# Optimization experiments

Hardware: AMD Instinct MI355X
Metric: run time of the kernel (lower is better)

Reference implementation:

```python
import jax, jax.numpy as jnp
import numpy as np

BS = 16; N_PER = 1024; N = BS * N_PER; K = 9; E = N * K
H = 128; NODE_D = 64; EDGE_D = 16; RBF_DIM = 20; R_CUT = 1.0; L = 4; SF = 0.1


def setup_inputs():
    ks = jax.random.split(jax.random.key(0), 24)
    X = jax.random.normal(ks[0], (N, 3), dtype=jnp.float32) * 0.5
    node_attr = jax.random.normal(ks[1], (N, NODE_D), dtype=jnp.float32)
    edge_attr = jax.random.normal(ks[2], (E, EDGE_D), dtype=jnp.float32)
    idx = jnp.arange(N, dtype=jnp.int32)
    bid = idx // N_PER
    Seg = ((idx % N_PER) >= (N_PER // 2)).astype(jnp.int32)
    row = jnp.repeat(idx, K)
    col = (row // N_PER) * N_PER + jax.random.randint(ks[3], (E,), 0, N_PER, dtype=jnp.int32)
    edges = jnp.stack([row, col])

    def g(k, shape, fan):
        return jax.random.normal(k, shape, dtype=jnp.float32) * (1.0 / float(np.sqrt(fan)))

    MI = 2 * H + RBF_DIM + EDGE_D  # message MLP input dim
    return {
        'X': X, 'node_attr': node_attr, 'edge_attr': edge_attr,
        'W_in1': g(ks[4], (NODE_D, H), NODE_D), 'b_in1': jnp.zeros((H,), jnp.float32),
        'W_in2': g(ks[5], (H, H), H), 'b_in2': jnp.zeros((H,), jnp.float32),
        'We1': g(ks[6], (L, MI, H), MI), 'be1': jnp.zeros((L, H), jnp.float32),
        'We2': g(ks[7], (L, H, H), H), 'be2': jnp.zeros((L, H), jnp.float32),
        'Wv': g(ks[8], (L, H, H), H), 'Wvv': g(ks[9], (L, H, H), H),
        'Wh1': g(ks[10], (L, 2 * H, H), 2 * H), 'bh1': jnp.zeros((L, H), jnp.float32),
        'Wh2': g(ks[11], (L, H, H), H), 'bh2': jnp.zeros((L, H), jnp.float32),
        'Wi1': g(ks[12], (L, H, H), H), 'bi1': jnp.zeros((L, H), jnp.float32),
        'Wi2': g(ks[13], (L, H, H), H), 'bi2': jnp.zeros((L, H), jnp.float32),
        'Wgv1': g(ks[14], (H, H), H), 'Wgv2': g(ks[15], (H, H), H),
        'Wg1': g(ks[16], (2 * H, H), 2 * H), 'bg1': jnp.zeros((H,), jnp.float32),
        'Wg2': g(ks[17], (H, 2 * H), H), 'bg2': jnp.zeros((2 * H,), jnp.float32),
        'Wf': g(ks[18], (H, 9), H),
        'edges': edges, 'Seg': Seg, 'bid': bid,
    }


def _fwd(X, node_attr, edge_attr, W_in1, b_in1, W_in2, b_in2, We1, be1, We2, be2, Wv, Wvv, Wh1, bh1, Wh2, bh2, Wi1, bi1, Wi2, bi2, Wgv1, Wgv2, Wg1, bg1, Wg2, bg2, Wf, edges, Seg, bid):
    silu = jax.nn.silu
    row, col = edges[0], edges[1]
    nseg = 2 * BS
    seg_id = bid * 2 + Seg  # (complex, receptor/ligand) segment id
    # coord2radial + Bessel RBF with cosine cutoff
    diff = X[row] - X[col]
    norm = jnp.sqrt(jnp.sum(diff * diff, axis=-1)) + 1e-8
    unit = diff / norm[:, None]
    freqs = jnp.arange(1, RBF_DIM + 1, dtype=X.dtype) * (jnp.pi / R_CUT)
    rbf = jnp.sin(norm[:, None] * freqs[None, :]) / norm[:, None]
    cut = 0.5 * (jnp.cos(jnp.pi * jnp.clip(norm, 0.0, R_CUT) / R_CUT) + 1.0)
    rbf = rbf * cut[:, None]
    # in_conv
    h = silu(node_attr @ W_in1 + b_in1) @ W_in2 + b_in2
    v = jnp.zeros((N, H, 3), dtype=h.dtype)
    counts = jax.ops.segment_sum(jnp.ones((N,), dtype=h.dtype), seg_id, num_segments=nseg)
    opp = bid * 2 + (1 - Seg)  # opposite-molecule segment per node
    for i in range(L):
        # PINN message passing (PaiNN-style equivariant layer)
        m_in = jnp.concatenate([h[row], h[col], rbf, edge_attr], axis=-1)
        m = silu(m_in @ We1[i] + be1[i]) @ We2[i] + be2[i]  # [E, H]
        agg = jax.ops.segment_sum(m, row, num_segments=N)
        h_intra = h + silu(jnp.concatenate([h, agg], axis=-1) @ Wh1[i] + bh1[i]) @ Wh2[i] + bh2[i]
        v_msg = (m @ Wv[i])[:, :, None] * unit[:, None, :] + (m @ Wvv[i])[:, :, None] * v[col]
        v = v + jax.ops.segment_sum(v_msg, row, num_segments=N)
        # cross receptor<->ligand softmax attention: (H_a @ H_b.T).mean(1) == H_a @ mean(H_b)
        mean_h = jax.ops.segment_sum(h_intra, seg_id, num_segments=nseg) / counts[:, None]
        score = jnp.sum(h_intra * mean_h[opp], axis=-1)
        smax = jax.ops.segment_max(score, seg_id, num_segments=nseg)
        ex = jnp.exp(score - smax[seg_id])
        w = ex / jax.ops.segment_sum(ex, seg_id, num_segments=nseg)[seg_id]
        gated = h_intra * w[:, None]
        h = h_intra + silu(gated @ Wi1[i] + bi1[i]) @ Wi2[i] + bi2[i]
    # gated equivariant block
    v1 = jnp.einsum('nhc,hk->nkc', v, Wgv1)
    v2 = jnp.einsum('nhc,hk->nkc', v, Wgv2)
    v2n = jnp.sqrt(jnp.sum(v2 * v2, axis=-1) + 1e-8)
    mix = silu(jnp.concatenate([h, v2n], axis=-1) @ Wg1 + bg1) @ Wg2 + bg2
    h, bgate = mix[:, :H], mix[:, H:]
    v = v1 * bgate[:, :, None]
    # final_conv + per-(complex, molecule) pooled prediction vectors [2*BS, 9, 3]
    pv = jnp.einsum('nhc,ho->noc', v * h[:, :, None], Wf)
    pred = jax.ops.segment_sum(pv.reshape(N, 27), seg_id, num_segments=nseg).reshape(nseg, 9, 3)
    # kron/outer-product quadratic surface params: A [., 3, 3], b [., 3]
    A = (pred[:, 0, :, None] * pred[:, 1, None, :] + pred[:, 3, :, None] * pred[:, 2, None, :]
         + pred[:, 4, :, None] * pred[:, 5, None, :] + pred[:, 7, :, None] * pred[:, 6, None, :]) / (SF * SF)
    bvec = pred[:, 8] / SF
    return jnp.concatenate([A, bvec[:, :, None]], axis=2)  # [2*BS, 3, 4]


def reference(X, node_attr, edge_attr, W_in1, b_in1, W_in2, b_in2, We1, be1, We2, be2, Wv, Wvv, Wh1, bh1, Wh2, bh2, Wi1, bi1, Wi2, bi2, Wgv1, Wgv2, Wg1, bg1, Wg2, bg2, Wf, edges, Seg, bid):
    return _fwd(X, node_attr, edge_attr, W_in1, b_in1, W_in2, b_in2, We1, be1, We2, be2, Wv, Wvv, Wh1, bh1, Wh2, bh2, Wi1, bi1, Wi2, bi2, Wgv1, Wgv2, Wg1, bg1, Wg2, bg2, Wf, edges, Seg, bid)
```

## Files before the change

### kernel.cpp

```cpp
#include <hip/hip_runtime.h>
#include <math.h>

#define NN 16384
#define NE 147456
#define NSEGS 32
#define HD 128
#define RBF_D 20
#define EDGE_DD 16
#define NODE_DD 64
#define NLAYER 4
#define PI_F 3.14159265358979323846f


typedef __attribute__((ext_vector_type(8))) short v8s;
typedef __attribute__((ext_vector_type(4))) float v4f;
typedef __attribute__((ext_vector_type(8))) unsigned short v8u;

__device__ __forceinline__ unsigned short f2bf(float f) {
  union { float f; unsigned int u; } x; x.f = f;
  unsigned int u = x.u;
  return (unsigned short)((u + 0x7FFFu + ((u >> 16) & 1u)) >> 16);
}
__device__ __forceinline__ float bf2f(unsigned short b) {
  union { unsigned int u; float f; } x; x.u = ((unsigned int)b) << 16; return x.f;
}
__device__ __forceinline__ void split8(float4 a, float4 b, v8u& hi, v8u& lo) {
  float v[8] = {a.x, a.y, a.z, a.w, b.x, b.y, b.z, b.w};
#pragma unroll
  for (int i = 0; i < 8; i++) {
    unsigned short h = f2bf(v[i]);
    hi[i] = h;
    lo[i] = f2bf(v[i] - bf2f(h));
  }
}
__device__ __forceinline__ float silu_f(float v) { return v / (1.f + expf(-v)); }

struct WDesc { const float* src; const float* src2; unsigned short* hi; unsigned short* lo;
               int K; int N; int Kp; int ld; };
struct WDescs { WDesc d[48]; };
__global__ void wconv_k(WDescs ds) {
  WDesc d = ds.d[blockIdx.y];
  int idx = blockIdx.x * 256 + threadIdx.x;
  if (idx >= d.N * d.Kp) return;
  int n = idx / d.Kp, k = idx - n * d.Kp;
  const float* s = d.src; int nn = n;
  if (d.src2 && n >= 128) { s = d.src2; nn = n - 128; }
  float v = (k < d.K) ? s[(size_t)k * d.ld + nn] : 0.f;
  unsigned short h = f2bf(v);
  d.hi[idx] = h;
  d.lo[idx] = f2bf(v - bf2f(h));
}

__global__ void wcomb_k(const float* __restrict__ We2, const float* __restrict__ Wv,
                        const float* __restrict__ Wvv, float* __restrict__ Wc) {
  int l = blockIdx.z, which = blockIdx.y, xb = blockIdx.x;
  const float* A = We2 + (size_t)l * 128 * 128;
  const float* B = (which ? Wvv : Wv) + (size_t)l * 128 * 128;
  float* D = Wc + ((size_t)(which * NLAYER + l)) * 128 * 128;
  int n = threadIdx.x & 127, r2 = threadIdx.x >> 7;
#pragma unroll
  for (int i = 0; i < 8; i++) {
    int k1 = xb * 16 + r2 * 8 + i;
    float s = 0.f;
    for (int j = 0; j < 128; j++) s += A[k1 * 128 + j] * B[j * 128 + n];
    D[(size_t)k1 * 128 + n] = s;
  }
}
__global__ void bcomb_k(const float* __restrict__ be2, const float* __restrict__ Wv,
                        const float* __restrict__ Wvv, const float* __restrict__ be1,
                        float* __restrict__ bcv, float* __restrict__ bcvv,
                        float* __restrict__ b9, float* __restrict__ bx) {
  int l = blockIdx.x, n = threadIdx.x;
  const float* b = be2 + l * 128;
  float sv = 0.f, svv = 0.f;
  for (int j = 0; j < 128; j++) {
    sv  += b[j] * Wv[(size_t)l * 16384 + j * 128 + n];
    svv += b[j] * Wvv[(size_t)l * 16384 + j * 128 + n];
  }
  bcv[l * 128 + n] = sv; bcvv[l * 128 + n] = svv; b9[l * 128 + n] = 9.f * b[n];
  bx[l * 256 + n] = be1[l * 128 + n]; bx[l * 256 + 128 + n] = 0.f;
}

constexpr int LDS_S = 40;

template<int BM, int AMODE, int OUTM, int RESM>
__global__ __launch_bounds__(256, 2)
void mgemm_k(const float* A0f, const unsigned short* Ah0, const unsigned short* Al0,
             const unsigned short* __restrict__ Wth, const unsigned short* __restrict__ Wtl,
             int Kp, const float* __restrict__ bias, const float* __restrict__ resf,
             float* Cf, int ldc, unsigned short* Ch, unsigned short* Cl, int lda)
{
  constexpr int MT = BM / 32;
  __shared__ unsigned short Ah[BM * LDS_S], Al[BM * LDS_S];
  __shared__ unsigned short Bh[128 * LDS_S], Bl[128 * LDS_S];
  const int tid = threadIdx.x;
  const int m0 = blockIdx.x * BM;
  const int coff = blockIdx.y * 128;
  const int w = tid >> 6, lane = tid & 63;
  const int lm = lane & 15, kq = lane >> 4;
  const int wm = (w >> 1) * (BM / 2);
  const int wn = (w & 1) * 64;

  v4f acc[MT][4];
#pragma unroll
  for (int i = 0; i < MT; i++)
#pragma unroll
    for (int j = 0; j < 4; j++) acc[i][j] = (v4f){0.f, 0.f, 0.f, 0.f};

  const int KT = Kp >> 5;
  for (int kt = 0; kt < KT; kt++) {
#pragma unroll
    for (int i = 0; i < BM / 64; i++) {
      int m = i * 64 + (tid >> 2);
      int k8 = (tid & 3) * 8;
      int gk = kt * 32 + k8, gm = m0 + m;
      v8u hi, lo;
      if constexpr (AMODE == 1) {
        hi = *(const v8u*)&Ah0[(size_t)gm * 128 + gk];
        lo = *(const v8u*)&Al0[(size_t)gm * 128 + gk];
      } else {
        float4 a = *(const float4*)&A0f[(size_t)gm * lda + gk];
        float4 b = *(const float4*)&A0f[(size_t)gm * lda + gk + 4];
        split8(a, b, hi, lo);
      }
      *(v8u*)&Ah[m * LDS_S + k8] = hi;
      *(v8u*)&Al[m * LDS_S + k8] = lo;
    }
#pragma unroll
    for (int i = 0; i < 2; i++) {
      int f = i * 256 + tid;
      int n = f >> 2, k8 = (f & 3) * 8;
      size_t g = (size_t)(coff + n) * Kp + kt * 32 + k8;
      *(v8u*)&Bh[n * LDS_S + k8] = *(const v8u*)&Wth[g];
      *(v8u*)&Bl[n * LDS_S + k8] = *(const v8u*)&Wtl[g];
    }
    __syncthreads();
    v8s afh[MT], afl[MT];
#pragma unroll
    for (int mi = 0; mi < MT; mi++) {
      int r = wm + mi * 16 + lm;
      afh[mi] = *(v8s*)&Ah[r * LDS_S + kq * 8];
      afl[mi] = *(v8s*)&Al[r * LDS_S + kq * 8];
    }
#pragma unroll
    for (int ni = 0; ni < 4; ni++) {
      int r = wn + ni * 16 + lm;
      v8s bh = *(v8s*)&Bh[r * LDS_S + kq * 8];
      v8s bl = *(v8s*)&Bl[r * LDS_S + kq * 8];
#pragma unroll
      for (int mi = 0; mi < MT; mi++) {
        acc[mi][ni] = __builtin_amdgcn_mfma_f32_16x16x32_bf16(afh[mi], bh, acc[mi][ni], 0, 0, 0);
        acc[mi][ni] = __builtin_amdgcn_mfma_f32_16x16x32_bf16(afl[mi], bh, acc[mi][ni], 0, 0, 0);
        acc[mi][ni] = __builtin_amdgcn_mfma_f32_16x16x32_bf16(afh[mi], bl, acc[mi][ni], 0, 0, 0);
      }
    }
    __syncthreads();
  }
#pragma unroll
  for (int mi = 0; mi < MT; mi++) {
#pragma unroll
    for (int r = 0; r < 4; r++) {
      int mrow = m0 + wm + mi * 16 + kq * 4 + r;
#pragma unroll
      for (int ni = 0; ni < 4; ni++) {
        int ncol = coff + wn + ni * 16 + lm;
        float v = acc[mi][ni][r];
        if constexpr (RESM == 3) v += bias[ncol] * resf[mrow];
        else { if (bias) v += bias[ncol]; }
        if constexpr (OUTM == 0) Cf[(size_t)mrow * ldc + ncol] = v;
        else if constexpr (OUTM == 1) {
          unsigned short h = f2bf(v);
          Ch[(size_t)mrow * 128 + ncol] = h;
          Cl[(size_t)mrow * 128 + ncol] = f2bf(v - bf2f(h));
        } else {
          Ch[(size_t)mrow * 128 + ncol] = f2bf(v);
        }
      }
    }
  }
}

__device__ __forceinline__ float4 loadRE(const float* __restrict__ rbf,
                                         const float* __restrict__ ea, int m, int k4) {
  if (k4 < RBF_D) return *(const float4*)&rbf[(size_t)m * RBF_D + k4];
  if (k4 < RBF_D + EDGE_DD) return *(const float4*)&ea[(size_t)m * EDGE_DD + k4 - RBF_D];
  return make_float4(0.f, 0.f, 0.f, 0.f);
}

__global__ __launch_bounds__(256, 2)
void mrev_k(const float* __restrict__ rbf, const float* __restrict__ ea,
            const float* __restrict__ hrc, const float* __restrict__ unitv,
            const int* __restrict__ gcol,
            const unsigned short* __restrict__ W1h, const unsigned short* __restrict__ W1l,
            const unsigned short* __restrict__ W2h, const unsigned short* __restrict__ W2l,
            const float* __restrict__ bcvv,
            float* __restrict__ agg, float* __restrict__ U,
            unsigned short* __restrict__ mvvh)
{
  __shared__ unsigned short Ah[64 * LDS_S], Al[64 * LDS_S];
  __shared__ unsigned short Bh[128 * LDS_S], Bl[128 * LDS_S];
  __shared__ unsigned short Th[64 * 136], Tl[64 * 136];
  __shared__ float su[192];
  const int tid = threadIdx.x;
  const int m0 = blockIdx.x * 64;
  const int w = tid >> 6, lane = tid & 63;
  const int lm = lane & 15, kq = lane >> 4;
  const int wm = (w >> 1) * 32, wn = (w & 1) * 64;

  if (tid < 192) su[tid] = unitv[(size_t)m0 * 3 + tid];

  v4f acc[2][4];
#pragma unroll
  for (int i = 0; i < 2; i++)
#pragma unroll
    for (int j = 0; j < 4; j++) acc[i][j] = (v4f){0.f, 0.f, 0.f, 0.f};

  for (int kt = 0; kt < 2; kt++) {
    {
      int m = tid >> 2, k8 = (tid & 3) * 8;
      int gk = kt * 32 + k8, gm = m0 + m;
      v8u hi, lo;
      split8(loadRE(rbf, ea, gm, gk), loadRE(rbf, ea, gm, gk + 4), hi, lo);
      *(v8u*)&Ah[m * LDS_S + k8] = hi;
      *(v8u*)&Al[m * LDS_S + k8] = lo;
    }
#pragma unroll
    for (int i = 0; i < 2; i++) {
      int f = i * 256 + tid;
      int n = f >> 2, k8 = (f & 3) * 8;
      size_t g = (size_t)n * 64 + kt * 32 + k8;
      *(v8u*)&Bh[n * LDS_S + k8] = *(const v8u*)&W1h[g];
      *(v8u*)&Bl[n * LDS_S + k8] = *(const v8u*)&W1l[g];
    }
    __syncthreads();
    v8s afh[2], afl[2];
#pragma unroll
    for (int mi = 0; mi < 2; mi++) {
      int r = wm + mi * 16 + lm;
      afh[mi] = *(v8s*)&Ah[r * LDS_S + kq * 8];
      afl[mi] = *(v8s*)&Al[r * LDS_S + kq * 8];
    }
#pragma unroll
    for (int ni = 0; ni < 4; ni++) {
      int r = wn + ni * 16 + lm;
      v8s bh = *(v8s*)&Bh[r * LDS_S + kq * 8];
      v8s bl = *(v8s*)&Bl[r * LDS_S + kq * 8];
#pragma unroll
      for (int mi = 0; mi < 2; mi++) {
        acc[mi][ni] = __builtin_amdgcn_mfma_f32_16x16x32_bf16(afh[mi], bh, acc[mi][ni], 0, 0, 0);
        acc[mi][ni] = __builtin_amdgcn_mfma_f32_16x16x32_bf16(afl[mi], bh, acc[mi][ni], 0, 0, 0);
        acc[mi][ni] = __builtin_amdgcn_mfma_f32_16x16x32_bf16(afh[mi], bl, acc[mi][ni], 0, 0, 0);
      }
    }
    __syncthreads();
  }
#pragma unroll
  for (int mi = 0; mi < 2; mi++) {
#pragma unroll
    for (int r = 0; r < 4; r++) {
      int row = wm + mi * 16 + kq * 4 + r;
      int e = m0 + row;
      const float* pr = hrc + (size_t)(e / 9) * 256;
      const float* pc = hrc + (size_t)gcol[e] * 256 + 128;
#pragma unroll
      for (int ni = 0; ni < 4; ni++) {
        int nc = wn + ni * 16 + lm;
        float v = silu_f(acc[mi][ni][r] + pr[nc] + pc[nc]);
        unsigned short h = f2bf(v);
        Th[row * 136 + nc] = h;
        Tl[row * 136 + nc] = f2bf(v - bf2f(h));
      }
    }
  }
  __syncthreads();
  {
    const size_t P = (size_t)NN * 128;
    int nfirst = m0 / 9;
#pragma unroll
    for (int it = 0; it < 4; it++) {
      int idx = it * 256 + tid;
      int ln = idx >> 7, c = idx & 127;
      int n = nfirst + ln;
      int r0 = n * 9 - m0, r1 = r0 + 9;
      if (r0 < 0) r0 = 0;
      if (r1 > 64) r1 = 64;
      float s = 0.f, u0 = 0.f, u1 = 0.f, u2 = 0.f;
      for (int r = r0; r < r1; r++) {
        float m = bf2f(Th[r * 136 + c]) + bf2f(Tl[r * 136 + c]);
        s += m;
        u0 += su[r * 3 + 0] * m;
        u1 += su[r * 3 + 1] * m;
        u2 += su[r * 3 + 2] * m;
      }
      if (r0 < r1) {
        size_t b = (size_t)n * 128 + c;
        atomicAdd(&agg[b], s);
        atomicAdd(&U[b], u0);
        atomicAdd(&U[P + b], u1);
        atomicAdd(&U[2 * P + b], u2);
      }
    }
  }
  v4f acc2[2][4];
#pragma unroll
  for (int i = 0; i < 2; i++)
#pragma unroll
    for (int j = 0; j < 4; j++) acc2[i][j] = (v4f){0.f, 0.f, 0.f, 0.f};
  for (int kt = 0; kt < 4; kt++) {
#pragma unroll
    for (int i = 0; i < 2; i++) {
      int f = i * 256 + tid;
      int n = f >> 2, k8 = (f & 3) * 8;
      size_t g = (size_t)n * 128 + kt * 32 + k8;
      *(v8u*)&Bh[n * LDS_S + k8] = *(const v8u*)&W2h[g];
      *(v8u*)&Bl[n * LDS_S + k8] = *(const v8u*)&W2l[g];
    }
    __syncthreads();
    v8s afh[2], afl[2];
#pragma unroll
    for (int mi = 0; mi < 2; mi++) {
      int r = wm + mi * 16 + lm;
      afh[mi] = *(v8s*)&Th[r * 136 + kt * 32 + kq * 8];
      afl[mi] = *(v8s*)&Tl[r * 136 + kt * 32 + kq * 8];
    }
#pragma unroll
    for (int ni = 0; ni < 4; ni++) {
      int r = wn + ni * 16 + lm;
      v8s bh = *(v8s*)&Bh[r * LDS_S + kq * 8];
      v8s bl = *(v8s*)&Bl[r * LDS_S + kq * 8];
#pragma unroll
      for (int mi = 0; mi < 2; mi++) {
        acc2[mi][ni] = __builtin_amdgcn_mfma_f32_16x16x32_bf16(afh[mi], bh, acc2[mi][ni], 0, 0, 0);
        acc2[mi][ni] = __builtin_amdgcn_mfma_f32_16x16x32_bf16(afl[mi], bh, acc2[mi][ni], 0, 0, 0);
        acc2[mi][ni] = __builtin_amdgcn_mfma_f32_16x16x32_bf16(afh[mi], bl, acc2[mi][ni], 0, 0, 0);
      }
    }
    __syncthreads();
  }
#pragma unroll
  for (int mi = 0; mi < 2; mi++) {
#pragma unroll
    for (int r = 0; r < 4; r++) {
      int e = m0 + wm + mi * 16 + kq * 4 + r;
#pragma unroll
      for (int ni = 0; ni < 4; ni++) {
        int nc = wn + ni * 16 + lm;
        mvvh[(size_t)e * 128 + nc] = f2bf(acc2[mi][ni][r] + bcvv[nc]);
      }
    }
  }
}

template<int AMODE, int OUTM, int RESM>
__global__ __launch_bounds__(256, 2)
void mlp2_k(const float* A0f, const float* A1f,
            const unsigned short* Ah0, const unsigned short* Al0,
            const unsigned short* __restrict__ W1h, const unsigned short* __restrict__ W1l,
            int k1p, const float* __restrict__ b1,
            const unsigned short* __restrict__ W2h, const unsigned short* __restrict__ W2l,
            const float* __restrict__ b2,
            const float* resf, const unsigned short* resh, const unsigned short* resl,
            float* Cf, int ldc, unsigned short* Ch, unsigned short* Cl, int lda)
{
  __shared__ unsigned short Ah[64 * LDS_S], Al[64 * LDS_S];
  __shared__ unsigned short Bh[128 * LDS_S], Bl[128 * LDS_S];
  __shared__ unsigned short Th[64 * 136], Tl[64 * 136];
  const int tid = threadIdx.x;
  const int m0 = blockIdx.x * 64;
  const int w = tid >> 6, lane = tid & 63;
  const int lm = lane & 15, kq = lane >> 4;
  const int wm = (w >> 1) * 32, wn = (w & 1) * 64;

  v4f acc[2][4];
#pragma unroll
  for (int i = 0; i < 2; i++)
#pragma unroll
    for (int j = 0; j < 4; j++) acc[i][j] = (v4f){0.f, 0.f, 0.f, 0.f};

  for (int kt = 0; kt < (k1p >> 5); kt++) {
    {
      int m = tid >> 2, k8 = (tid & 3) * 8;
      int gk = kt * 32 + k8, gm = m0 + m;
      v8u hi, lo;
      if constexpr (AMODE == 3) {
        if (gk < 128) {
          hi = *(const v8u*)&Ah0[(size_t)gm * 128 + gk];
          lo = *(const v8u*)&Al0[(size_t)gm * 128 + gk];
        } else {
          float4 a = *(const float4*)&A1f[(size_t)gm * 128 + gk - 128];
          float4 b = *(const float4*)&A1f[(size_t)gm * 128 + gk - 124];
          split8(a, b, hi, lo);
        }
      } else {
        float4 a = *(const float4*)&A0f[(size_t)gm * lda + gk];
        float4 b = *(const float4*)&A0f[(size_t)gm * lda + gk + 4];
        if constexpr (AMODE == 4) {
          float s = A1f[gm];
          a.x *= s; a.y *= s; a.z *= s; a.w *= s;
          b.x *= s; b.y *= s; b.z *= s; b.w *= s;
        }
        split8(a, b, hi, lo);
      }
      *(v8u*)&Ah[m * LDS_S + k8] = hi;
      *(v8u*)&Al[m * LDS_S + k8] = lo;
    }
#pragma unroll
    for (int i = 0; i < 2; i++) {
      int f = i * 256 + tid;
      int n = f >> 2, k8 = (f & 3) * 8;
      size_t g = (size_t)n * k1p + kt * 32 + k8;
      *(v8u*)&Bh[n * LDS_S + k8] = *(const v8u*)&W1h[g];
      *(v8u*)&Bl[n * LDS_S + k8] = *(const v8u*)&W1l[g];
    }
    __syncthreads();
    v8s afh[2], afl[2];
#pragma unroll
    for (int mi = 0; mi < 2; mi++) {
      int r = wm + mi * 16 + lm;
      afh[mi] = *(v8s*)&Ah[r * LDS_S + kq * 8];
      afl[mi] = *(v8s*)&Al[r * LDS_S + kq * 8];
    }
#pragma unroll
    for (int ni = 0; ni < 4; ni++) {
      int r = wn + ni * 16 + lm;
      v8s bh = *(v8s*)&Bh[r * LDS_S + kq * 8];
      v8s bl = *(v8s*)&Bl[r * LDS_S + kq * 8];
#pragma unroll
      for (int mi = 0; mi < 2; mi++) {
        acc[mi][ni] = __builtin_amdgcn_mfma_f32_16x16x32_bf16(afh[mi], bh, acc[mi][ni], 0, 0, 0);
        acc[mi][ni] = __builtin_amdgcn_mfma_f32_16x16x32_bf16(afl[mi], bh, acc[mi][ni], 0, 0, 0);
        acc[mi][ni] = __builtin_amdgcn_mfma_f32_16x16x32_bf16(afh[mi], bl, acc[mi][ni], 0, 0, 0);
      }
    }
    __syncthreads();
  }
#pragma unroll
  for (int mi = 0; mi < 2; mi++) {
#pragma unroll
    for (int r = 0; r < 4; r++) {
      int row = wm + mi * 16 + kq * 4 + r;
#pragma unroll
      for (int ni = 0; ni < 4; ni++) {
        int col = wn + ni * 16 + lm;
        float v = silu_f(acc[mi][ni][r] + b1[col]);
        unsigned short h = f2bf(v);
        Th[row * 136 + col] = h;
        Tl[row * 136 + col] = f2bf(v - bf2f(h));
      }
    }
  }
  __syncthreads();
  const int coff2 = blockIdx.y * 128;
  v4f acc2[2][4];
#pragma unroll
  for (int i = 0; i < 2; i++)
#pragma unroll
    for (int j = 0; j < 4; j++) acc2[i][j] = (v4f){0.f, 0.f, 0.f, 0.f};
  for (int kt = 0; kt < 4; kt++) {
#pragma unroll
    for (int i = 0; i < 2; i++) {
      int f = i * 256 + tid;
      int n = f >> 2, k8 = (f & 3) * 8;
      size_t g = (size_t)(coff2 + n) * 128 + kt * 32 + k8;
      *(v8u*)&Bh[n * LDS_S + k8] = *(const v8u*)&W2h[g];
      *(v8u*)&Bl[n * LDS_S + k8] = *(const v8u*)&W2l[g];
    }
    __syncthreads();
    v8s afh[2], afl[2];
#pragma unroll
    for (int mi = 0; mi < 2; mi++) {
      int r = wm + mi * 16 + lm;
      afh[mi] = *(v8s*)&Th[r * 136 + kt * 32 + kq * 8];
      afl[mi] = *(v8s*)&Tl[r * 136 + kt * 32 + kq * 8];
    }
#pragma unroll
    for (int ni = 0; ni < 4; ni++) {
      int r = wn + ni * 16 + lm;
      v8s bh = *(v8s*)&Bh[r * LDS_S + kq * 8];
      v8s bl = *(v8s*)&Bl[r * LDS_S + kq * 8];
#pragma unroll
      for (int mi = 0; mi < 2; mi++) {
        acc2[mi][ni] = __builtin_amdgcn_mfma_f32_16x16x32_bf16(afh[mi], bh, acc2[mi][ni], 0, 0, 0);
        acc2[mi][ni] = __builtin_amdgcn_mfma_f32_16x16x32_bf16(afl[mi], bh, acc2[mi][ni], 0, 0, 0);
        acc2[mi][ni] = __builtin_amdgcn_mfma_f32_16x16x32_bf16(afh[mi], bl, acc2[mi][ni], 0, 0, 0);
      }
    }
    __syncthreads();
  }
#pragma unroll
  for (int mi = 0; mi < 2; mi++) {
#pragma unroll
    for (int r = 0; r < 4; r++) {
      int mrow = m0 + wm + mi * 16 + kq * 4 + r;
#pragma unroll
      for (int ni = 0; ni < 4; ni++) {
        int ncol = coff2 + wn + ni * 16 + lm;
        float v = acc2[mi][ni][r];
        if (b2) v += b2[ncol];
        if constexpr (RESM == 1) v += resf[(size_t)mrow * 128 + ncol];
        if constexpr (RESM == 2) v += bf2f(resh[(size_t)mrow * 128 + ncol]) + bf2f(resl[(size_t)mrow * 128 + ncol]);
        if constexpr (OUTM == 0) Cf[(size_t)mrow * ldc + ncol] = v;
        else {
          unsigned short h = f2bf(v);
          Ch[(size_t)mrow * 128 + ncol] = h;
          Cl[(size_t)mrow * 128 + ncol] = f2bf(v - bf2f(h));
        }
      }
    }
  }
}

__global__ void edge_geom_k(const float* __restrict__ X, const int* __restrict__ row,
                            const int* __restrict__ col,
                            float* __restrict__ unitv, float* __restrict__ rbf) {
  int e = blockIdx.x * 256 + threadIdx.x;
  if (e >= NE) return;
  int r = row[e], c = col[e];
  float dx = X[r * 3 + 0] - X[c * 3 + 0];
  float dy = X[r * 3 + 1] - X[c * 3 + 1];
  float dz = X[r * 3 + 2] - X[c * 3 + 2];
  float norm = sqrtf(dx * dx + dy * dy + dz * dz) + 1e-8f;
  float inv = 1.f / norm;
  unitv[e * 3 + 0] = dx * inv;
  unitv[e * 3 + 1] = dy * inv;
  unitv[e * 3 + 2] = dz * inv;
  float cl = fminf(norm, 1.0f);
  float cut = 0.5f * (cosf(PI_F * cl) + 1.0f);
  float s = cut * inv;
#pragma unroll
  for (int j = 0; j < RBF_D; j++) rbf[(size_t)e * RBF_D + j] = sinf(norm * (float)(j + 1) * PI_F) * s;
}

__global__ void sup_k(const float* __restrict__ unitv, float* __restrict__ sup) {
  int n = blockIdx.x * 256 + threadIdx.x;
  if (n >= NN) return;
  float q0 = 0.f, q1 = 0.f, q2 = 0.f;
#pragma unroll
  for (int k = 0; k < 9; k++) {
    const float* u = &unitv[(size_t)(n * 9 + k) * 3];
    q0 += u[0]; q1 += u[1]; q2 += u[2];
  }
  sup[n] = q0; sup[NN + n] = q1; sup[2 * NN + n] = q2;
}

__global__ void vupd_k(const float* __restrict__ vold, const float* __restrict__ t1,
                       const unsigned short* __restrict__ mvvh,
                       const int* __restrict__ col, float* __restrict__ vnew) {
  const size_t P = (size_t)NN * 128;
  int t = blockIdx.x * 256 + threadIdx.x;
  int n = t >> 7, hh = t & 127;
  size_t b = (size_t)n * 128 + hh;
  float a0 = vold[b] + t1[b];
  float a1 = vold[P + b] + t1[P + b];
  float a2 = vold[2 * P + b] + t1[2 * P + b];
#pragma unroll
  for (int k = 0; k < 9; k++) {
    int e = n * 9 + k;
    int ce = col[e];
    float mvv = bf2f(mvvh[(size_t)e * 128 + hh]);
    size_t cb = (size_t)ce * 128 + hh;
    a0 += mvv * vold[cb];
    a1 += mvv * vold[P + cb];
    a2 += mvv * vold[2 * P + cb];
  }
  vnew[b] = a0; vnew[P + b] = a1; vnew[2 * P + b] = a2;
}

__global__ void meanp_k(const float* __restrict__ hintra, float* __restrict__ meanp) {
  int q = blockIdx.x, s = blockIdx.y, c = threadIdx.x;
  const float* p = hintra + ((size_t)s * 512 + q * 64) * 128 + c;
  float a = 0.f;
  for (int r = 0; r < 64; r++) a += p[(size_t)r * 128];
  meanp[(s * 8 + q) * 128 + c] = a;
}
__global__ void score2_k(const float* __restrict__ hintra, const float* __restrict__ meanp,
                         float* __restrict__ score) {
  int lane = threadIdx.x & 63;
  int n = blockIdx.x * 4 + (threadIdx.x >> 6);
  int opp = (n >> 9) ^ 1;
  const float* mp = meanp + opp * 1024;
  float mh0 = 0.f, mh1 = 0.f;
#pragma unroll
  for (int q = 0; q < 8; q++) { mh0 += mp[q * 128 + lane]; mh1 += mp[q * 128 + lane + 64]; }
  const float* hp = hintra + (size_t)n * 128;
  float v = hp[lane] * mh0 + hp[lane + 64] * mh1;
#pragma unroll
  for (int off = 32; off > 0; off >>= 1) v += __shfl_down(v, off, 64);
  if (lane == 0) score[n] = v * (1.f / 512.f);
}
__global__ void softmax_k(const float* __restrict__ score, float* __restrict__ w) {
  __shared__ float red[512];
  int s = blockIdx.x, t = threadIdx.x;
  float sc = score[s * 512 + t];
  red[t] = sc;
  __syncthreads();
  for (int off = 256; off > 0; off >>= 1) {
    if (t < off) red[t] = fmaxf(red[t], red[t + off]);
    __syncthreads();
  }
  float mx = red[0];
  __syncthreads();
  float ex = expf(sc - mx);
  red[t] = ex;
  __syncthreads();
  for (int off = 256; off > 0; off >>= 1) {
    if (t < off) red[t] += red[t + off];
    __syncthreads();
  }
  w[s * 512 + t] = ex / red[0];
}

__global__ void v2n_k(const float* __restrict__ v12, float* __restrict__ v2n) {
  const size_t P = (size_t)NN * 256;
  int t = blockIdx.x * 256 + threadIdx.x;
  int n = t >> 7, h = t & 127;
  size_t b = (size_t)n * 256 + 128 + h;
  float a = v12[b], c = v12[P + b], d = v12[2 * P + b];
  v2n[t] = sqrtf(a * a + c * c + d * d + 1e-8f);
}

__global__ __launch_bounds__(256)
void pv_k(const float* __restrict__ v12, const float* __restrict__ mix,
          const float* __restrict__ Wf, float* __restrict__ pred) {
  __shared__ float sg[8][128];
  __shared__ float pr[8][32];
  const size_t P = (size_t)NN * 256;
  int t = threadIdx.x;
  int nb = blockIdx.x * 8;
#pragma unroll
  for (int i = 0; i < 4; i++) {
    int idx = i * 256 + t;
    int nn = idx >> 7, hh = idx & 127;
    const float* mxp = mix + (size_t)(nb + nn) * 256;
    sg[nn][hh] = mxp[hh] * mxp[128 + hh];
  }
  __syncthreads();
  int nn = t >> 5, j = t & 31;
  float acc = 0.f;
  if (j < 27) {
    int o = j / 3, c = j - o * 3;
    const float* vp = v12 + (size_t)c * P + (size_t)(nb + nn) * 256;
    for (int hh = 0; hh < 128; hh++) acc += sg[nn][hh] * vp[hh] * Wf[hh * 9 + o];
  }
  pr[nn][j] = acc;
  __syncthreads();
  if (t < 32) {
    float s = pr[0][t] + pr[1][t] + pr[2][t] + pr[3][t] +
              pr[4][t] + pr[5][t] + pr[6][t] + pr[7][t];
    if (t < 27) atomicAdd(&pred[(nb >> 9) * 27 + t], s);
  }
}

__global__ void out_k(const float* __restrict__ pred, float* __restrict__ out) {
  int s = threadIdx.x;
  if (s >= NSEGS) return;
  float p[27];
#pragma unroll
  for (int j = 0; j < 27; j++) p[j] = pred[s * 27 + j];
#pragma unroll
  for (int i = 0; i < 3; i++) {
#pragma unroll
    for (int j = 0; j < 3; j++) {
      float a = p[0 * 3 + i] * p[1 * 3 + j] + p[3 * 3 + i] * p[2 * 3 + j]
              + p[4 * 3 + i] * p[5 * 3 + j] + p[7 * 3 + i] * p[6 * 3 + j];
      out[s * 12 + i * 4 + j] = a * 100.f;
    }
    out[s * 12 + i * 4 + 3] = p[8 * 3 + i] * 10.f;
  }
}

extern "C" void kernel_launch(void* const* d_in, const int* in_sizes, int n_in,
                              void* d_out, int out_size, void* d_ws, size_t ws_size,
                              hipStream_t stream) {
  const float* X         = (const float*)d_in[0];
  const float* node_attr = (const float*)d_in[1];
  const float* edge_attr = (const float*)d_in[2];
  const float* W_in1 = (const float*)d_in[3];
  const float* b_in1 = (const float*)d_in[4];
  const float* W_in2 = (const float*)d_in[5];
  const float* b_in2 = (const float*)d_in[6];
  const float* We1 = (const float*)d_in[7];
  const float* be1 = (const float*)d_in[8];
  const float* We2 = (const float*)d_in[9];
  const float* be2 = (const float*)d_in[10];
  const float* Wv  = (const float*)d_in[11];
  const float* Wvv = (const float*)d_in[12];
  const float* Wh1 = (const float*)d_in[13];
  const float* bh1 = (const float*)d_in[14];
  const float* Wh2 = (const float*)d_in[15];
  const float* bh2 = (const float*)d_in[16];
  const float* Wi1 = (const float*)d_in[17];
  const float* bi1 = (const float*)d_in[18];
  const float* Wi2 = (const float*)d_in[19];
  const float* bi2 = (const float*)d_in[20];
  const float* Wgv1 = (const float*)d_in[21];
  const float* Wgv2 = (const float*)d_in[22];
  const float* Wg1 = (const float*)d_in[23];
  const float* bg1 = (const float*)d_in[24];
  const float* Wg2 = (const float*)d_in[25];
  const float* bg2 = (const float*)d_in[26];
  const float* Wf  = (const float*)d_in[27];
  const int* edges = (const int*)d_in[28];
  const int* rowp = edges;
  const int* colp = edges + NE;
  float* out = (float*)d_out;

  char* ws = (char*)d_ws;
  size_t o = 0;
  auto ab = [&](size_t bytes) { char* p = ws + o; o += (bytes + 255) & ~(size_t)255; return p; };
  float* unitv  = (float*)ab((size_t)NE * 3 * 4);
  float* rbf    = (float*)ab((size_t)NE * RBF_D * 4);
  float* va     = (float*)ab((size_t)NN * 384 * 4);
  float* vb     = (float*)ab((size_t)NN * 384 * 4);
  unsigned short* mvvh = (unsigned short*)ab((size_t)NE * 128 * 2);
  float* hrc    = (float*)ab((size_t)NN * 256 * 4);
  float* U      = (float*)ab((size_t)3 * NN * 128 * 4);
  float* agg    = (float*)ab((size_t)NN * 128 * 4);
  float* sup    = (float*)ab((size_t)3 * NN * 4);
  float* hintra = (float*)ab((size_t)NN * 128 * 4);
  unsigned short* hbh = (unsigned short*)ab((size_t)NN * 128 * 2);
  unsigned short* hbl = (unsigned short*)ab((size_t)NN * 128 * 2);
  float* meanp  = (float*)ab(NSEGS * 8 * 128 * 4);
  float* scoreb = (float*)ab(NN * 4);
  float* wgt    = (float*)ab(NN * 4);
  float* pred   = (float*)ab(NSEGS * 27 * 4);
  float* Wc     = (float*)ab((size_t)2 * NLAYER * 128 * 128 * 4);
  float* bcv    = (float*)ab(NLAYER * 128 * 4);
  float* bcvv   = (float*)ab(NLAYER * 128 * 4);
  float* b9     = (float*)ab(NLAYER * 128 * 4);
  float* bx     = (float*)ab(NLAYER * 256 * 4);
  unsigned short* wt = (unsigned short*)ab(4 * 1024 * 1024);
  float* v12  = (float*)mvvh;
  float* mixb = (float*)U;

  size_t wo = 0;
  auto walloc = [&](size_t n) { unsigned short* p = wt + wo; wo += n; return p; };
  WDescs wd{};
  int wcnt = 0;
  auto addw = [&](const float* src, const float* src2, int K, int N, int Kp, int ld) {
    size_t sz = (size_t)N * Kp;
    unsigned short* hi = walloc(sz);
    unsigned short* lo = walloc(sz);
    wd.d[wcnt] = WDesc{src, src2, hi, lo, K, N, Kp, ld};
    return wcnt++;
  };
  int iWin1 = addw(W_in1, nullptr, 64, 128, 64, 128);
  int iWin2 = addw(W_in2, nullptr, 128, 128, 128, 128);
  int iWe1rc[NLAYER], iWe1re[NLAYER], iWe2[NLAYER], iWcv[NLAYER], iWcvv[NLAYER],
      iWh1[NLAYER], iWh2[NLAYER], iWi1[NLAYER], iWi2[NLAYER];
  for (int i = 0; i < NLAYER; i++) {
    const float* Wl = We1 + (size_t)i * 292 * 128;
    iWe1rc[i] = addw(Wl, Wl + 128 * 128, 128, 256, 128, 128);
    iWe1re[i] = addw(Wl + 256 * 128, nullptr, 36, 128, 64, 128);
    iWe2[i]   = addw(We2 + (size_t)i * 16384, nullptr, 128, 128, 128, 128);
    iWcv[i]   = addw(Wc + (size_t)i * 16384, nullptr, 128, 128, 128, 128);
    iWcvv[i]  = addw(Wc + (size_t)(NLAYER + i) * 16384, nullptr, 128, 128, 128, 128);
    iWh1[i]   = addw(Wh1 + (size_t)i * 256 * 128, nullptr, 256, 128, 256, 128);
    iWh2[i]   = addw(Wh2 + (size_t)i * 16384, nullptr, 128, 128, 128, 128);
    iWi1[i]   = addw(Wi1 + (size_t)i * 16384, nullptr, 128, 128, 128, 128);
    iWi2[i]   = addw(Wi2 + (size_t)i * 16384, nullptr, 128, 128, 128, 128);
  }
  int iWg1   = addw(Wg1, nullptr, 256, 128, 256, 128);
  int iWg2   = addw(Wg2, nullptr, 128, 256, 128, 256);
  int iWgv12 = addw(Wgv1, Wgv2, 128, 256, 128, 128);

  hipMemsetAsync(va, 0, (size_t)NN * 384 * sizeof(float), stream);
  hipMemsetAsync(pred, 0, NSEGS * 27 * sizeof(float), stream);

  wcomb_k<<<dim3(8, 2, NLAYER), 256, 0, stream>>>(We2, Wv, Wvv, Wc);
  bcomb_k<<<NLAYER, 128, 0, stream>>>(be2, Wv, Wvv, be1, bcv, bcvv, b9, bx);
  wconv_k<<<dim3(128, wcnt), 256, 0, stream>>>(wd);
  edge_geom_k<<<NE / 256, 256, 0, stream>>>(X, rowp, colp, unitv, rbf);
  sup_k<<<NN / 256, 256, 0, stream>>>(unitv, sup);

  auto WH = [&](int idx) { return wd.d[idx].hi; };
  auto WL = [&](int idx) { return wd.d[idx].lo; };

  mlp2_k<0, 1, 0><<<dim3(NN / 64, 1), 256, 0, stream>>>(
      node_attr, nullptr, nullptr, nullptr,
      WH(iWin1), WL(iWin1), 64, b_in1, WH(iWin2), WL(iWin2), b_in2,
      nullptr, nullptr, nullptr, nullptr, 128, hbh, hbl, NODE_DD);

  float* vcur = va;
  float* vnxt = vb;
  for (int i = 0; i < NLAYER; i++) {
    hipMemsetAsync(U, 0, (size_t)4 * NN * 128 * sizeof(float), stream);
    mgemm_k<64, 1, 0, 0><<<dim3(NN / 64, 2), 256, 0, stream>>>(
        nullptr, hbh, hbl, WH(iWe1rc[i]), WL(iWe1rc[i]), 128,
        bx + i * 256, nullptr, hrc, 256, nullptr, nullptr, 0);
    mrev_k<<<NE / 64, 256, 0, stream>>>(rbf, edge_attr, hrc, unitv, colp,
        WH(iWe1re[i]), WL(iWe1re[i]), WH(iWcvv[i]), WL(iWcvv[i]),
        bcvv + i * 128, agg, U, mvvh);
    mgemm_k<64, 0, 0, 0><<<dim3(NN / 64, 1), 256, 0, stream>>>(
        agg, nullptr, nullptr, WH(iWe2[i]), WL(iWe2[i]), 128,
        b9 + i * 128, nullptr, agg, 128, nullptr, nullptr, 128);
    mlp2_k<3, 0, 2><<<dim3(NN / 64, 1), 256, 0, stream>>>(
        nullptr, agg, hbh, hbl,
        WH(iWh1[i]), WL(iWh1[i]), 256, bh1 + i * 128, WH(iWh2[i]), WL(iWh2[i]), bh2 + i * 128,
        nullptr, hbh, hbl, hintra, 128, nullptr, nullptr, 0);
    meanp_k<<<dim3(8, NSEGS), 128, 0, stream>>>(hintra, meanp);
    score2_k<<<NN / 4, 256, 0, stream>>>(hintra, meanp, scoreb);
    softmax_k<<<NSEGS, 512, 0, stream>>>(scoreb, wgt);
    mgemm_k<64, 0, 0, 3><<<dim3(3 * NN / 64, 1), 256, 0, stream>>>(
        U, nullptr, nullptr, WH(iWcv[i]), WL(iWcv[i]), 128,
        bcv + i * 128, sup, U, 128, nullptr, nullptr, 128);
    vupd_k<<<NN * 128 / 256, 256, 0, stream>>>(vcur, U, mvvh, colp, vnxt);
    { float* t = vcur; vcur = vnxt; vnxt = t; }
    mlp2_k<4, 1, 1><<<dim3(NN / 64, 1), 256, 0, stream>>>(
        hintra, wgt, nullptr, nullptr,
        WH(iWi1[i]), WL(iWi1[i]), 128, bi1 + i * 128, WH(iWi2[i]), WL(iWi2[i]), bi2 + i * 128,
        hintra, nullptr, nullptr, nullptr, 128, hbh, hbl, 128);
  }

  mgemm_k<64, 0, 0, 0><<<dim3(3 * NN / 64, 2), 256, 0, stream>>>(
      vcur, nullptr, nullptr, WH(iWgv12), WL(iWgv12), 128,
      nullptr, nullptr, v12, 256, nullptr, nullptr, 128);
  v2n_k<<<NN * 128 / 256, 256, 0, stream>>>(v12, agg);
  mlp2_k<3, 0, 0><<<dim3(NN / 64, 2), 256, 0, stream>>>(
      nullptr, agg, hbh, hbl,
      WH(iWg1), WL(iWg1), 256, bg1, WH(iWg2), WL(iWg2), bg2,
      nullptr, nullptr, nullptr, mixb, 256, nullptr, nullptr, 0);
  pv_k<<<NN / 8, 256, 0, stream>>>(v12, mixb, Wf, pred);
  out_k<<<1, 64, 0, stream>>>(pred, out);
}
```

Before: 1.137 ms.

## Read mrev weight fragments directly from global memory and raise occupancy

In the edge message kernel, the weight B-fragments are now loaded straight from global memory (served by L1/L2) instead of being staged through shared-memory tiles. The A staging buffers are aliased onto the Th/Tl scratch, and the now-unneeded barriers in the second GEMM loop are removed. Together with the launch bound raised to 4 blocks per CU, this cuts LDS footprint and synchronization so more blocks can be resident. The trade-off is more global/cache traffic per wave for the weights, and a risk that the shared-memory aliasing or missing barriers cause ordering hazards.

```diff
diff --git a/kernel.cpp b/kernel.cpp
--- a/kernel.cpp
+++ b/kernel.cpp
@@ -187,7 +187,7 @@
   return make_float4(0.f, 0.f, 0.f, 0.f);
 }
 
-__global__ __launch_bounds__(256, 2)
+__global__ __launch_bounds__(256, 4)
 void mrev_k(const float* __restrict__ rbf, const float* __restrict__ ea,
             const float* __restrict__ hrc, const float* __restrict__ unitv,
             const int* __restrict__ gcol,
@@ -197,10 +197,10 @@
             float* __restrict__ agg, float* __restrict__ U,
             unsigned short* __restrict__ mvvh)
 {
-  __shared__ unsigned short Ah[64 * LDS_S], Al[64 * LDS_S];
-  __shared__ unsigned short Bh[128 * LDS_S], Bl[128 * LDS_S];
   __shared__ unsigned short Th[64 * 136], Tl[64 * 136];
   __shared__ float su[192];
+  unsigned short* Ah = Th;
+  unsigned short* Al = Th + 64 * LDS_S;
   const int tid = threadIdx.x;
   const int m0 = blockIdx.x * 64;
   const int w = tid >> 6, lane = tid & 63;
@@ -224,14 +224,6 @@
       *(v8u*)&Ah[m * LDS_S + k8] = hi;
       *(v8u*)&Al[m * LDS_S + k8] = lo;
     }
-#pragma unroll
-    for (int i = 0; i < 2; i++) {
-      int f = i * 256 + tid;
-      int n = f >> 2, k8 = (f & 3) * 8;
-      size_t g = (size_t)n * 64 + kt * 32 + k8;
-      *(v8u*)&Bh[n * LDS_S + k8] = *(const v8u*)&W1h[g];
-      *(v8u*)&Bl[n * LDS_S + k8] = *(const v8u*)&W1l[g];
-    }
     __syncthreads();
     v8s afh[2], afl[2];
 #pragma unroll
@@ -242,9 +234,9 @@
     }
 #pragma unroll
     for (int ni = 0; ni < 4; ni++) {
-      int r = wn + ni * 16 + lm;
-      v8s bh = *(v8s*)&Bh[r * LDS_S + kq * 8];
-      v8s bl = *(v8s*)&Bl[r * LDS_S + kq * 8];
+      int n = wn + ni * 16 + lm;
+      v8s bh = *(const v8s*)&W1h[(size_t)n * 64 + kt * 32 + kq * 8];
+      v8s bl = *(const v8s*)&W1l[(size_t)n * 64 + kt * 32 + kq * 8];
 #pragma unroll
       for (int mi = 0; mi < 2; mi++) {
         acc[mi][ni] = __builtin_amdgcn_mfma_f32_16x16x32_bf16(afh[mi], bh, acc[mi][ni], 0, 0, 0);
@@ -307,15 +299,6 @@
 #pragma unroll
     for (int j = 0; j < 4; j++) acc2[i][j] = (v4f){0.f, 0.f, 0.f, 0.f};
   for (int kt = 0; kt < 4; kt++) {
-#pragma unroll
-    for (int i = 0; i < 2; i++) {
-      int f = i * 256 + tid;
-      int n = f >> 2, k8 = (f & 3) * 8;
-      size_t g = (size_t)n * 128 + kt * 32 + k8;
-      *(v8u*)&Bh[n * LDS_S + k8] = *(const v8u*)&W2h[g];
-      *(v8u*)&Bl[n * LDS_S + k8] = *(const v8u*)&W2l[g];
-    }
-    __syncthreads();
     v8s afh[2], afl[2];
 #pragma unroll
     for (int mi = 0; mi < 2; mi++) {
@@ -325,9 +308,9 @@
     }
 #pragma unroll
     for (int ni = 0; ni < 4; ni++) {
-      int r = wn + ni * 16 + lm;
-      v8s bh = *(v8s*)&Bh[r * LDS_S + kq * 8];
-      v8s bl = *(v8s*)&Bl[r * LDS_S + kq * 8];
+      int n = wn + ni * 16 + lm;
+      v8s bh = *(const v8s*)&W2h[(size_t)n * 128 + kt * 32 + kq * 8];
+      v8s bl = *(const v8s*)&W2l[(size_t)n * 128 + kt * 32 + kq * 8];
 #pragma unroll
       for (int mi = 0; mi < 2; mi++) {
         acc2[mi][ni] = __builtin_amdgcn_mfma_f32_16x16x32_bf16(afh[mi], bh, acc2[mi][ni], 0, 0, 0);
@@ -335,7 +318,6 @@
         acc2[mi][ni] = __builtin_amdgcn_mfma_f32_16x16x32_bf16(afh[mi], bl, acc2[mi][ni], 0, 0, 0);
       }
     }
-    __syncthreads();
   }
 #pragma unroll
   for (int mi = 0; mi < 2; mi++) {
```

Measured after the change: 1.142 ms. No clear change (+0.4%).
